# Performance work log

Measured on AMD Instinct MI355X. Metric: run time of the kernel, lower is better.

## Reference

```python
import jax, jax.numpy as jnp
import numpy as np


def setup_inputs() -> dict:
    key = jax.random.key(0)
    k1, k2, k3, k4 = jax.random.split(key, 4)
    B, T, S, D = 32, 512, 1024, 1024
    inp = jax.random.normal(k1, (B, T, D), dtype=jnp.float32)
    ctx = jax.random.normal(k2, (B, S, D), dtype=jnp.float32)
    W_in = jax.random.normal(k3, (D, D), dtype=jnp.float32) * (1.0 / np.sqrt(D))
    W_out = jax.random.normal(k4, (D, 2 * D), dtype=jnp.float32) * (1.0 / np.sqrt(2 * D))
    return {"input": inp, "context": ctx, "W_in": W_in, "W_out": W_out}


def reference(input, context, W_in, W_out):
    # GlobalAttention, attn_type='general', no mask, no coverage, tgt_len > 1.
    B, T, D = input.shape
    S = context.shape[1]
    # score: (W_in h_t) . h_s   -> [B, T, S]
    h_t = jnp.einsum('btd,ed->bte', input, W_in)           # linear_in (no bias)
    align = jnp.einsum('btd,bsd->bts', h_t, context)
    align_vectors = jax.nn.softmax(align, axis=-1)          # [B, T, S]
    # weighted sum of context
    c = jnp.einsum('bts,bsd->btd', align_vectors, context)  # [B, T, D]
    # concat [c, input] -> linear_out (no bias for 'general') -> tanh
    concat_c = jnp.concatenate([c, input], axis=-1)          # [B, T, 2D]
    attn_h = jnp.tanh(jnp.einsum('btf,df->btd', concat_c, W_out))
    # not one_step: transpose to [T, B, ...]
    attn_h = jnp.transpose(attn_h, (1, 0, 2))
    align_vectors = jnp.transpose(align_vectors, (1, 0, 2))
    return attn_h, align_vectors
```

## Files before the change

### kernel.cpp

```cpp
#include <hip/hip_runtime.h>
#include <hip/hip_bf16.h>


typedef short bf16x8 __attribute__((ext_vector_type(8)));
typedef float f32x4 __attribute__((ext_vector_type(4)));
typedef unsigned short us;

#define NB 32
#define NT_ 512
#define NS 1024
#define ND 1024

__device__ inline us f2bf(float x) {
  unsigned u = __float_as_uint(x);
  u += 0x7FFFu + ((u >> 16) & 1u);
  return (us)(u >> 16);
}
__device__ inline float bf2f(us h) { return __uint_as_float(((unsigned)h) << 16); }

__device__ inline void store_split(us* __restrict__ hi, us* __restrict__ lo, size_t idx, float v) {
  us h = f2bf(v);
  hi[idx] = h;
  lo[idx] = f2bf(v - bf2f(h));
}

__global__ void ga_split(const float* __restrict__ src, us* __restrict__ hi,
                         us* __restrict__ lo, long n) {
  long i0 = ((long)blockIdx.x * blockDim.x + threadIdx.x) * 4;
  long stride = (long)gridDim.x * blockDim.x * 4;
  for (long i = i0; i < n; i += stride) {
    float4 v = *reinterpret_cast<const float4*>(src + i);
    ushort4 h, l;
    h.x = f2bf(v.x); l.x = f2bf(v.x - bf2f(h.x));
    h.y = f2bf(v.y); l.y = f2bf(v.y - bf2f(h.y));
    h.z = f2bf(v.z); l.z = f2bf(v.z - bf2f(h.z));
    h.w = f2bf(v.w); l.w = f2bf(v.w - bf2f(h.w));
    *reinterpret_cast<ushort4*>(hi + i) = h;
    *reinterpret_cast<ushort4*>(lo + i) = l;
  }
}

__global__ void ga_cvt(const float* __restrict__ src, us* __restrict__ dst, long n) {
  long i0 = ((long)blockIdx.x * blockDim.x + threadIdx.x) * 4;
  long stride = (long)gridDim.x * blockDim.x * 4;
  for (long i = i0; i < n; i += stride) {
    float4 v = *reinterpret_cast<const float4*>(src + i);
    ushort4 h;
    h.x = f2bf(v.x); h.y = f2bf(v.y); h.z = f2bf(v.z); h.w = f2bf(v.w);
    *reinterpret_cast<ushort4*>(dst + i) = h;
  }
}

__global__ void ga_transpose_split(const float* __restrict__ ctx, us* __restrict__ tHi,
                                   us* __restrict__ tLo) {
  __shared__ float tile[64][65];
  int s0 = blockIdx.x << 6, d0 = blockIdx.y << 6, b = blockIdx.z;
  const float* src = ctx + (size_t)b * NS * ND;
  int tid = threadIdx.x;
#pragma unroll
  for (int i = 0; i < 16; ++i) {
    int lin = (i << 8) + tid;
    int r = lin >> 6, c = lin & 63;
    tile[r][c] = src[(size_t)(s0 + r) * ND + d0 + c];
  }
  __syncthreads();
  us* oH = tHi + (size_t)b * ND * NS;
  us* oL = tLo + (size_t)b * ND * NS;
#pragma unroll
  for (int i = 0; i < 16; ++i) {
    int lin = (i << 8) + tid;
    int dr = lin >> 6, sc = lin & 63;
    float v = tile[sc][dr];
    size_t o = (size_t)(d0 + dr) * NS + s0 + sc;
    us h = f2bf(v);
    oH[o] = h;
    oL[o] = f2bf(v - bf2f(h));
  }
}

__global__ __launch_bounds__(256) void ga_softmax(float* __restrict__ al,
                                                  us* __restrict__ pHi, us* __restrict__ pLo) {
  int row = blockIdx.x;
  int tid = threadIdx.x;
  float* p = al + (size_t)row * NS;
  float4 v = *reinterpret_cast<const float4*>(p + (tid << 2));
  float m = fmaxf(fmaxf(v.x, v.y), fmaxf(v.z, v.w));
#pragma unroll
  for (int off = 32; off; off >>= 1) m = fmaxf(m, __shfl_xor(m, off));
  __shared__ float rmax[4], rsum[4];
  int wv = tid >> 6, ln = tid & 63;
  if (ln == 0) rmax[wv] = m;
  __syncthreads();
  m = fmaxf(fmaxf(rmax[0], rmax[1]), fmaxf(rmax[2], rmax[3]));
  float4 e;
  e.x = __expf(v.x - m); e.y = __expf(v.y - m);
  e.z = __expf(v.z - m); e.w = __expf(v.w - m);
  float s = e.x + e.y + e.z + e.w;
#pragma unroll
  for (int off = 32; off; off >>= 1) s += __shfl_xor(s, off);
  if (ln == 0) rsum[wv] = s;
  __syncthreads();
  s = rsum[0] + rsum[1] + rsum[2] + rsum[3];
  float inv = 1.0f / s;
  e.x *= inv; e.y *= inv; e.z *= inv; e.w *= inv;
  *reinterpret_cast<float4*>(p + (tid << 2)) = e;
  int t = row >> 5, b = row & 31;
  size_t o = ((size_t)b * NT_ + t) * NS + (tid << 2);
  ushort4 h, l;
  h.x = f2bf(e.x); l.x = f2bf(e.x - bf2f(h.x));
  h.y = f2bf(e.y); l.y = f2bf(e.y - bf2f(h.y));
  h.z = f2bf(e.z); l.z = f2bf(e.z - bf2f(h.z));
  h.w = f2bf(e.w); l.w = f2bf(e.w - bf2f(h.w));
  *reinterpret_cast<ushort4*>(pHi + o) = h;
  *reinterpret_cast<ushort4*>(pLo + o) = l;
}

__device__ inline void gload16(const us* g, void* l) {
  __builtin_amdgcn_global_load_lds((const __attribute__((address_space(1))) unsigned int*)g,
                                   (__attribute__((address_space(3))) unsigned int*)l, 16, 0, 0);
}

__device__ inline f32x4 mfma16(bf16x8 a, bf16x8 b, f32x4 c) {
  return __builtin_amdgcn_mfma_f32_16x16x32_bf16(a, b, c, 0, 0, 0);
}


#define VM4 asm volatile("s_waitcnt vmcnt(4)" ::: "memory")
#define VM0 asm volatile("s_waitcnt vmcnt(0)" ::: "memory")

#define STG_A(T, H) do {                                                           \
    int s3_ = (T) >> 4;                                                            \
    const us* ga_ = (MODE == 3)                                                    \
        ? ((s3_ == 0) ? pA0 : (s3_ == 1) ? pA1 : (s3_ == 2) ? pA2 : pA3)           \
        : ((s3_ == 2) ? pA1 : pA0);                                                \
    const us* g_ = ga_ + ((long)((T) & 15) << 6) + ((H) ? aOff1 : aOff0);          \
    char* d_ = lb + (((T) & 1) << 16) + ((H) << 14) + (tid << 4);                  \
    gload16(g_, d_);                                                               \
    gload16(g_ + ald64, d_ + 8192);                                                \
  } while (0)

#define STG_B(T, H) do {                                                           \
    int s3_ = (T) >> 4;                                                            \
    const us* gb_ = (MODE == 3) ? ((s3_ >= 2) ? pB2 : pB0)                         \
                                : ((s3_ == 1) ? pB1 : pB0);                        \
    const us* g_ = gb_ + ((long)((T) & 15) << 6) + ((H) ? bOff1 : bOff0);          \
    char* d_ = lb + (((T) & 1) << 16) + 32768 + ((H) << 14) + (tid << 4);          \
    gload16(g_, d_);                                                               \
    gload16(g_ + bld64, d_ + 8192);                                                \
  } while (0)

#define RD_A(BP, QM) do {                                                          \
    const char* p_ = (BP) + aRd + ((QM) << 13);                                    \
    _Pragma("unroll") for (int m_ = 0; m_ < 4; ++m_) {                             \
      a[m_][0] = *(const bf16x8*)(p_ + (m_ << 11) + colx0);                        \
      a[m_][1] = *(const bf16x8*)(p_ + (m_ << 11) + colx1);                        \
    }                                                                              \
  } while (0)

#define RD_B(BP, ARR, QN) do {                                                     \
    const char* p_ = (BP) + bRd + ((QN) << 12);                                    \
    _Pragma("unroll") for (int n_ = 0; n_ < 2; ++n_) {                             \
      ARR[n_][0] = *(const bf16x8*)(p_ + (n_ << 11) + colx0);                      \
      ARR[n_][1] = *(const bf16x8*)(p_ + (n_ << 11) + colx1);                      \
    }                                                                              \
  } while (0)

#define MM(QM, QN, ARR)                                                            \
  _Pragma("unroll") for (int ks_ = 0; ks_ < 2; ++ks_)                              \
  _Pragma("unroll") for (int m_ = 0; m_ < 4; ++m_)                                 \
  _Pragma("unroll") for (int n_ = 0; n_ < 2; ++n_)                                 \
    acc[(QM) * 4 + m_][(QN) * 2 + n_] =                                            \
        mfma16(a[m_][ks_], ARR[n_][ks_], acc[(QM) * 4 + m_][(QN) * 2 + n_])

#define PHX(RDS, STGS, TAILV, QM, QN, ARR) do {                                    \
    RDS;                                                                           \
    STGS;                                                                          \
    __builtin_amdgcn_s_barrier();                                                  \
    asm volatile("s_waitcnt lgkmcnt(0)" ::: "memory");                             \
    __builtin_amdgcn_sched_barrier(0);                                             \
    __builtin_amdgcn_s_setprio(1);                                                 \
    MM(QM, QN, ARR);                                                               \
    __builtin_amdgcn_s_setprio(0);                                                 \
    TAILV;                                                                         \
    __builtin_amdgcn_s_barrier();                                                  \
  } while (0)

template <int MODE>
__global__ __launch_bounds__(512, 2) void ga_g8(
    const us* __restrict__ Ahi, const us* __restrict__ Alo,
    const us* __restrict__ A2hi, const us* __restrict__ A2lo,
    const us* __restrict__ Bhi, const us* __restrict__ Blo,
    void* __restrict__ out0, void* __restrict__ out1,
    int K, int lda, int ldb, long astride, long bstride) {
  __shared__ __align__(16) char lds[131072];
  char* lb = lds;
  const int NTILES = K >> 6;
  const int NIT = NTILES >> 1;
  const int tid = threadIdx.x;
  const int lane = tid & 63;
  const int fr = lane & 15;
  const int wv = tid >> 6;
  const int wr = wv >> 2, wc = wv & 3;
  const int rowA = blockIdx.x << 8, colB = blockIdx.y << 8;
  const int bz = blockIdx.z;

  const us* pA0 = Ahi + (size_t)bz * astride + (size_t)rowA * lda;
  const us* pA1 = Alo + (size_t)bz * astride + (size_t)rowA * lda;
  const us* pA2 = (MODE == 3) ? A2hi + (size_t)rowA * lda : nullptr;
  const us* pA3 = (MODE == 3) ? A2lo + (size_t)rowA * lda : nullptr;
  const us* pB0 = Bhi + (size_t)bz * bstride + (size_t)colB * ldb;
  const us* pB1 = (MODE == 3) ? nullptr : Blo + (size_t)bz * bstride + (size_t)colB * ldb;
  const us* pB2 = (MODE == 3) ? pB0 + 1024 : nullptr;

  const int arow = tid >> 3;
  const long swe = (long)(((tid & 7) ^ (arow & 7)) << 3);
  const long aOff0 = (long)arow * lda + swe;
  const long aOff1 = aOff0 + 128L * lda;
  const long ald64 = 64L * lda;
  const long bOff0 = (long)arow * ldb + swe;
  const long bOff1 = bOff0 + 128L * ldb;
  const long bld64 = 64L * ldb;

  const int l16 = ((lane >> 4) & 3) << 4;
  const int colx0 = l16 ^ ((fr & 7) << 4);
  const int colx1 = colx0 ^ 64;
  const int aRd = (wr << 14) + (fr << 7);
  const int bRd = 32768 + ((wc >> 1) << 14) + ((wc & 1) << 13) + (fr << 7);
  const char* B0P = lb;
  const char* B1P = lb + 65536;

  bf16x8 a[4][2], b0[2][2], b1[2][2];
  f32x4 zero = {0.f, 0.f, 0.f, 0.f};
  f32x4 acc[8][4];
#pragma unroll
  for (int i = 0; i < 8; ++i)
#pragma unroll
    for (int k = 0; k < 4; ++k) acc[i][k] = zero;

  STG_A(0, 0); STG_A(0, 1); STG_B(0, 0); STG_B(0, 1);
  STG_B(1, 0); STG_B(1, 1);
  VM4;
  __builtin_amdgcn_s_barrier();

  for (int i = 0; i < NIT - 1; ++i) {
    const int X = i << 1;
    PHX({ RD_A(B0P, 0); RD_B(B0P, b0, 0); }, STG_A(X + 1, 0), , 0, 0, b0);
    PHX(RD_B(B0P, b1, 1),                    STG_A(X + 1, 1), , 0, 1, b1);
    PHX(RD_A(B0P, 1),                        STG_B(X + 2, 0), , 1, 1, b1);
    PHX(,                                    STG_B(X + 2, 1), VM4, 1, 0, b0);
    PHX({ RD_A(B1P, 0); RD_B(B1P, b0, 0); }, STG_A(X + 2, 0), , 0, 0, b0);
    PHX(RD_B(B1P, b1, 1),                    STG_A(X + 2, 1), , 0, 1, b1);
    PHX(RD_A(B1P, 1),                        STG_B(X + 3, 0), , 1, 1, b1);
    PHX(,                                    STG_B(X + 3, 1), VM4, 1, 0, b0);
  }
  {
    const int X = NTILES - 2;
    PHX({ RD_A(B0P, 0); RD_B(B0P, b0, 0); }, STG_A(X + 1, 0), , 0, 0, b0);
    PHX(RD_B(B0P, b1, 1),                    STG_A(X + 1, 1), , 0, 1, b1);
    PHX(RD_A(B0P, 1), , , 1, 1, b1);
    PHX(, , VM0, 1, 0, b0);
    PHX({ RD_A(B1P, 0); RD_B(B1P, b0, 0); }, , , 0, 0, b0);
    PHX(RD_B(B1P, b1, 1), , , 0, 1, b1);
    PHX(RD_A(B1P, 1), , , 1, 1, b1);
    PHX(, , , 1, 0, b0);
  }

#pragma unroll
  for (int mf = 0; mf < 8; ++mf)
#pragma unroll
    for (int nf = 0; nf < 4; ++nf)
#pragma unroll
      for (int j = 0; j < 4; ++j) {
        int r = rowA + (wr << 7) + (mf << 4) + (((lane >> 4) & 3) << 2) + j;
        int c = colB + (wc << 6) + (nf << 4) + fr;
        float v = acc[mf][nf][j];
        if constexpr (MODE == 0) {
          store_split((us*)out0, (us*)out1, (size_t)r * 1024 + c, v);
        } else if constexpr (MODE == 1) {
          ((float*)out0)[((size_t)r * NB + bz) * NS + c] = v;
        } else if constexpr (MODE == 2) {
          store_split((us*)out0, (us*)out1, ((size_t)bz * 512 + r) * 1024 + c, v);
        } else {
          int bb = r >> 9, tt2 = r & 511;
          ((float*)out0)[((size_t)tt2 * NB + bb) * ND + c] = tanhf(v);
        }
      }
}

extern "C" void kernel_launch(void* const* d_in, const int* in_sizes, int n_in,
                              void* d_out, int out_size, void* d_ws, size_t ws_size,
                              hipStream_t stream) {
  (void)in_sizes; (void)n_in; (void)out_size; (void)ws_size;
  const float* inp = (const float*)d_in[0];
  const float* ctx = (const float*)d_in[1];
  const float* Win = (const float*)d_in[2];
  const float* Wout = (const float*)d_in[3];
  float* out = (float*)d_out;

  char* w = (char*)d_ws;
  us* ctx_hi  = (us*)(w + 0);
  us* c_hi    = (us*)(w + 0);
  us* c_lo    = (us*)(w + 33554432);
  us* ctx_lo  = (us*)(w + 67108864);
  us* p_hi    = (us*)(w + 67108864);
  us* p_lo    = (us*)(w + 100663296);
  us* in_hi   = (us*)(w + 134217728);
  us* in_lo   = (us*)(w + 167772160);
  us* h_hi    = (us*)(w + 201326592);
  us* h_lo    = (us*)(w + 234881024);
  us* ctxT_lo = (us*)(w + 201326592);
  us* win_hi  = (us*)(w + 268435456);
  us* win_lo  = (us*)(w + 270532608);
  us* wout_b  = (us*)(w + 272629760);

  us* ctxT_hi = (us*)d_out;
  float* alignOut = out + 16777216;

  ga_split<<<2048, 256, 0, stream>>>(inp, in_hi, in_lo, 16777216L);
  ga_split<<<2048, 256, 0, stream>>>(ctx, ctx_hi, ctx_lo, 33554432L);
  ga_split<<<512, 256, 0, stream>>>(Win, win_hi, win_lo, 1048576L);
  ga_cvt<<<512, 256, 0, stream>>>(Wout, wout_b, 2097152L);

  ga_g8<0><<<dim3(64, 4, 1), 512, 0, stream>>>(in_hi, in_lo, nullptr, nullptr,
                                               win_hi, win_lo, h_hi, h_lo,
                                               3072, 1024, 1024, 0L, 0L);
  ga_g8<1><<<dim3(2, 4, 32), 512, 0, stream>>>(h_hi, h_lo, nullptr, nullptr,
                                               ctx_hi, ctx_lo, alignOut, nullptr,
                                               3072, 1024, 1024, 524288L, 1048576L);
  ga_transpose_split<<<dim3(16, 16, 32), 256, 0, stream>>>(ctx, ctxT_hi, ctxT_lo);
  ga_softmax<<<16384, 256, 0, stream>>>(alignOut, p_hi, p_lo);
  ga_g8<2><<<dim3(2, 4, 32), 512, 0, stream>>>(p_hi, p_lo, nullptr, nullptr,
                                               ctxT_hi, ctxT_lo, c_hi, c_lo,
                                               3072, 1024, 1024, 524288L, 1048576L);
  ga_g8<3><<<dim3(64, 4, 1), 512, 0, stream>>>(c_hi, c_lo, in_hi, in_lo,
                                               wout_b, nullptr, out, nullptr,
                                               4096, 1024, 2048, 0L, 0L);
}
```

Before: 619.9 us.

## Restructure GEMM main loop to a single-barrier phase schedule with compile-time strides

Rewrites the 8-phase GEMM mainloop so each phase has one barrier instead of two. The B fragments are kept in registers across a whole k-tile and reloaded only at the tile boundary, and the global-to-LDS staging is moved after the MFMA block with vmcnt waits. Strides and tile counts become compile-time constants per mode, which cuts 64-bit address arithmetic and registers. Launch bounds change from 2 to 1 block per SM, trading occupancy for register headroom. The reordered LDS reads and writes add a risk of ordering hazards between buffers.

```diff
diff --git a/kernel.cpp b/kernel.cpp
--- a/kernel.cpp
+++ b/kernel.cpp
@@ -124,7 +124,6 @@
   return __builtin_amdgcn_mfma_f32_16x16x32_bf16(a, b, c, 0, 0, 0);
 }
 
-
 #define VM4 asm volatile("s_waitcnt vmcnt(4)" ::: "memory")
 #define VM0 asm volatile("s_waitcnt vmcnt(0)" ::: "memory")
 
@@ -133,27 +132,27 @@
     const us* ga_ = (MODE == 3)                                                    \
         ? ((s3_ == 0) ? pA0 : (s3_ == 1) ? pA1 : (s3_ == 2) ? pA2 : pA3)           \
         : ((s3_ == 2) ? pA1 : pA0);                                                \
-    const us* g_ = ga_ + ((long)((T) & 15) << 6) + ((H) ? aOff1 : aOff0);          \
+    const us* g_ = ga_ + (((T) & 15) << 6) + ((H) ? 131072 : 0) + aOff0;           \
     char* d_ = lb + (((T) & 1) << 16) + ((H) << 14) + (tid << 4);                  \
     gload16(g_, d_);                                                               \
-    gload16(g_ + ald64, d_ + 8192);                                                \
+    gload16(g_ + 65536, d_ + 8192);                                                \
   } while (0)
 
 #define STG_B(T, H) do {                                                           \
     int s3_ = (T) >> 4;                                                            \
     const us* gb_ = (MODE == 3) ? ((s3_ >= 2) ? pB2 : pB0)                         \
                                 : ((s3_ == 1) ? pB1 : pB0);                        \
-    const us* g_ = gb_ + ((long)((T) & 15) << 6) + ((H) ? bOff1 : bOff0);          \
+    const us* g_ = gb_ + (((T) & 15) << 6) + ((H) ? (LDB << 7) : 0) + bOff0;       \
     char* d_ = lb + (((T) & 1) << 16) + 32768 + ((H) << 14) + (tid << 4);          \
     gload16(g_, d_);                                                               \
-    gload16(g_ + bld64, d_ + 8192);                                                \
-  } while (0)
-
-#define RD_A(BP, QM) do {                                                          \
+    gload16(g_ + (LDB << 6), d_ + 8192);                                           \
+  } while (0)
+
+#define RD_A(BP, ARR, QM) do {                                                     \
     const char* p_ = (BP) + aRd + ((QM) << 13);                                    \
     _Pragma("unroll") for (int m_ = 0; m_ < 4; ++m_) {                             \
-      a[m_][0] = *(const bf16x8*)(p_ + (m_ << 11) + colx0);                        \
-      a[m_][1] = *(const bf16x8*)(p_ + (m_ << 11) + colx1);                        \
+      ARR[m_][0] = *(const bf16x8*)(p_ + (m_ << 11) + colx0);                      \
+      ARR[m_][1] = *(const bf16x8*)(p_ + (m_ << 11) + colx1);                      \
     }                                                                              \
   } while (0)
 
@@ -165,37 +164,34 @@
     }                                                                              \
   } while (0)
 
-#define MM(QM, QN, ARR)                                                            \
+#define MM(QM, QN, AA, BB)                                                         \
+  _Pragma("unroll") for (int m_ = 0; m_ < 4; ++m_)                                 \
   _Pragma("unroll") for (int ks_ = 0; ks_ < 2; ++ks_)                              \
-  _Pragma("unroll") for (int m_ = 0; m_ < 4; ++m_)                                 \
   _Pragma("unroll") for (int n_ = 0; n_ < 2; ++n_)                                 \
     acc[(QM) * 4 + m_][(QN) * 2 + n_] =                                            \
-        mfma16(a[m_][ks_], ARR[n_][ks_], acc[(QM) * 4 + m_][(QN) * 2 + n_])
-
-#define PHX(RDS, STGS, TAILV, QM, QN, ARR) do {                                    \
+        mfma16(AA[m_][ks_], BB[n_][ks_], acc[(QM) * 4 + m_][(QN) * 2 + n_])
+
+#define PH(RDS, MMQ, POST) do {                                                    \
+    __builtin_amdgcn_s_barrier();                                                  \
     RDS;                                                                           \
-    STGS;                                                                          \
-    __builtin_amdgcn_s_barrier();                                                  \
-    asm volatile("s_waitcnt lgkmcnt(0)" ::: "memory");                             \
-    __builtin_amdgcn_sched_barrier(0);                                             \
     __builtin_amdgcn_s_setprio(1);                                                 \
-    MM(QM, QN, ARR);                                                               \
+    MMQ;                                                                           \
     __builtin_amdgcn_s_setprio(0);                                                 \
-    TAILV;                                                                         \
-    __builtin_amdgcn_s_barrier();                                                  \
+    POST;                                                                          \
   } while (0)
 
 template <int MODE>
-__global__ __launch_bounds__(512, 2) void ga_g8(
+__global__ __launch_bounds__(512, 1) void ga_gb(
     const us* __restrict__ Ahi, const us* __restrict__ Alo,
     const us* __restrict__ A2hi, const us* __restrict__ A2lo,
     const us* __restrict__ Bhi, const us* __restrict__ Blo,
     void* __restrict__ out0, void* __restrict__ out1,
-    int K, int lda, int ldb, long astride, long bstride) {
+    long astride, long bstride) {
+  constexpr int LDB = (MODE == 3) ? 2048 : 1024;
+  constexpr int NT = (MODE == 3) ? 64 : 48;
+  constexpr int NIT = NT >> 1;
   __shared__ __align__(16) char lds[131072];
   char* lb = lds;
-  const int NTILES = K >> 6;
-  const int NIT = NTILES >> 1;
   const int tid = threadIdx.x;
   const int lane = tid & 63;
   const int fr = lane & 15;
@@ -204,32 +200,28 @@
   const int rowA = blockIdx.x << 8, colB = blockIdx.y << 8;
   const int bz = blockIdx.z;
 
-  const us* pA0 = Ahi + (size_t)bz * astride + (size_t)rowA * lda;
-  const us* pA1 = Alo + (size_t)bz * astride + (size_t)rowA * lda;
-  const us* pA2 = (MODE == 3) ? A2hi + (size_t)rowA * lda : nullptr;
-  const us* pA3 = (MODE == 3) ? A2lo + (size_t)rowA * lda : nullptr;
-  const us* pB0 = Bhi + (size_t)bz * bstride + (size_t)colB * ldb;
-  const us* pB1 = (MODE == 3) ? nullptr : Blo + (size_t)bz * bstride + (size_t)colB * ldb;
+  const us* pA0 = Ahi + (size_t)bz * astride + (size_t)rowA * 1024;
+  const us* pA1 = Alo + (size_t)bz * astride + (size_t)rowA * 1024;
+  const us* pA2 = (MODE == 3) ? A2hi + (size_t)rowA * 1024 : nullptr;
+  const us* pA3 = (MODE == 3) ? A2lo + (size_t)rowA * 1024 : nullptr;
+  const us* pB0 = Bhi + (size_t)bz * bstride + (size_t)colB * LDB;
+  const us* pB1 = (MODE == 3) ? nullptr : Blo + (size_t)bz * bstride + (size_t)colB * LDB;
   const us* pB2 = (MODE == 3) ? pB0 + 1024 : nullptr;
 
   const int arow = tid >> 3;
-  const long swe = (long)(((tid & 7) ^ (arow & 7)) << 3);
-  const long aOff0 = (long)arow * lda + swe;
-  const long aOff1 = aOff0 + 128L * lda;
-  const long ald64 = 64L * lda;
-  const long bOff0 = (long)arow * ldb + swe;
-  const long bOff1 = bOff0 + 128L * ldb;
-  const long bld64 = 64L * ldb;
+  const int swe = ((tid & 7) ^ (arow & 7)) << 3;
+  const int aOff0 = arow * 1024 + swe;
+  const int bOff0 = arow * LDB + swe;
 
   const int l16 = ((lane >> 4) & 3) << 4;
   const int colx0 = l16 ^ ((fr & 7) << 4);
   const int colx1 = colx0 ^ 64;
   const int aRd = (wr << 14) + (fr << 7);
   const int bRd = 32768 + ((wc >> 1) << 14) + ((wc & 1) << 13) + (fr << 7);
-  const char* B0P = lb;
-  const char* B1P = lb + 65536;
-
-  bf16x8 a[4][2], b0[2][2], b1[2][2];
+  const char* BUF0 = lb;
+  const char* BUF1 = lb + 65536;
+
+  bf16x8 a4[4][2], b0[2][2], b1[2][2];
   f32x4 zero = {0.f, 0.f, 0.f, 0.f};
   f32x4 acc[8][4];
 #pragma unroll
@@ -237,33 +229,34 @@
 #pragma unroll
     for (int k = 0; k < 4; ++k) acc[i][k] = zero;
 
-  STG_A(0, 0); STG_A(0, 1); STG_B(0, 0); STG_B(0, 1);
-  STG_B(1, 0); STG_B(1, 1);
-  VM4;
+  STG_B(0, 0); STG_B(0, 1); STG_A(0, 0); STG_A(0, 1);
+  STG_B(1, 0); STG_B(1, 1); STG_A(1, 0);
+  VM0;
   __builtin_amdgcn_s_barrier();
+  RD_B(BUF0, b0, 0); RD_B(BUF0, b1, 1);
 
   for (int i = 0; i < NIT - 1; ++i) {
     const int X = i << 1;
-    PHX({ RD_A(B0P, 0); RD_B(B0P, b0, 0); }, STG_A(X + 1, 0), , 0, 0, b0);
-    PHX(RD_B(B0P, b1, 1),                    STG_A(X + 1, 1), , 0, 1, b1);
-    PHX(RD_A(B0P, 1),                        STG_B(X + 2, 0), , 1, 1, b1);
-    PHX(,                                    STG_B(X + 2, 1), VM4, 1, 0, b0);
-    PHX({ RD_A(B1P, 0); RD_B(B1P, b0, 0); }, STG_A(X + 2, 0), , 0, 0, b0);
-    PHX(RD_B(B1P, b1, 1),                    STG_A(X + 2, 1), , 0, 1, b1);
-    PHX(RD_A(B1P, 1),                        STG_B(X + 3, 0), , 1, 1, b1);
-    PHX(,                                    STG_B(X + 3, 1), VM4, 1, 0, b0);
-  }
-  {
-    const int X = NTILES - 2;
-    PHX({ RD_A(B0P, 0); RD_B(B0P, b0, 0); }, STG_A(X + 1, 0), , 0, 0, b0);
-    PHX(RD_B(B0P, b1, 1),                    STG_A(X + 1, 1), , 0, 1, b1);
-    PHX(RD_A(B0P, 1), , , 1, 1, b1);
-    PHX(, , VM0, 1, 0, b0);
-    PHX({ RD_A(B1P, 0); RD_B(B1P, b0, 0); }, , , 0, 0, b0);
-    PHX(RD_B(B1P, b1, 1), , , 0, 1, b1);
-    PHX(RD_A(B1P, 1), , , 1, 1, b1);
-    PHX(, , , 1, 0, b0);
-  }
+    PH(RD_A(BUF0, a4, 0), MM(0, 0, a4, b0), { STG_A(X + 1, 1); VM4; });
+    PH(,                  MM(0, 1, a4, b1), { STG_B(X + 2, 0); VM4; });
+    PH(RD_A(BUF0, a4, 1), MM(1, 0, a4, b0), { STG_B(X + 2, 1); VM4; });
+    PH(,                  MM(1, 1, a4, b1),
+       { RD_B(BUF1, b0, 0); RD_B(BUF1, b1, 1); STG_A(X + 2, 0); VM4; });
+    PH(RD_A(BUF1, a4, 0), MM(0, 0, a4, b0), { STG_A(X + 2, 1); VM4; });
+    PH(,                  MM(0, 1, a4, b1), { STG_B(X + 3, 0); VM4; });
+    PH(RD_A(BUF1, a4, 1), MM(1, 0, a4, b0), { STG_B(X + 3, 1); VM4; });
+    PH(,                  MM(1, 1, a4, b1),
+       { RD_B(BUF0, b0, 0); RD_B(BUF0, b1, 1); STG_A(X + 3, 0); VM4; });
+  }
+  PH(RD_A(BUF0, a4, 0), MM(0, 0, a4, b0), { STG_A(NT - 1, 1); VM4; });
+  PH(,                  MM(0, 1, a4, b1), {});
+  PH(RD_A(BUF0, a4, 1), MM(1, 0, a4, b0), { VM0; });
+  PH(,                  MM(1, 1, a4, b1),
+     { RD_B(BUF1, b0, 0); RD_B(BUF1, b1, 1); });
+  PH(RD_A(BUF1, a4, 0), MM(0, 0, a4, b0), {});
+  PH(,                  MM(0, 1, a4, b1), {});
+  PH(RD_A(BUF1, a4, 1), MM(1, 0, a4, b0), {});
+  PH(,                  MM(1, 1, a4, b1), {});
 
 #pragma unroll
   for (int mf = 0; mf < 8; ++mf)
@@ -321,18 +314,16 @@
   ga_split<<<512, 256, 0, stream>>>(Win, win_hi, win_lo, 1048576L);
   ga_cvt<<<512, 256, 0, stream>>>(Wout, wout_b, 2097152L);
 
-  ga_g8<0><<<dim3(64, 4, 1), 512, 0, stream>>>(in_hi, in_lo, nullptr, nullptr,
-                                               win_hi, win_lo, h_hi, h_lo,
-                                               3072, 1024, 1024, 0L, 0L);
-  ga_g8<1><<<dim3(2, 4, 32), 512, 0, stream>>>(h_hi, h_lo, nullptr, nullptr,
+  ga_gb<0><<<dim3(64, 4, 1), 512, 0, stream>>>(in_hi, in_lo, nullptr, nullptr,
+                                               win_hi, win_lo, h_hi, h_lo, 0L, 0L);
+  ga_gb<1><<<dim3(2, 4, 32), 512, 0, stream>>>(h_hi, h_lo, nullptr, nullptr,
                                                ctx_hi, ctx_lo, alignOut, nullptr,
-                                               3072, 1024, 1024, 524288L, 1048576L);
+                                               524288L, 1048576L);
   ga_transpose_split<<<dim3(16, 16, 32), 256, 0, stream>>>(ctx, ctxT_hi, ctxT_lo);
   ga_softmax<<<16384, 256, 0, stream>>>(alignOut, p_hi, p_lo);
-  ga_g8<2><<<dim3(2, 4, 32), 512, 0, stream>>>(p_hi, p_lo, nullptr, nullptr,
+  ga_gb<2><<<dim3(2, 4, 32), 512, 0, stream>>>(p_hi, p_lo, nullptr, nullptr,
                                                ctxT_hi, ctxT_lo, c_hi, c_lo,
-                                               3072, 1024, 1024, 524288L, 1048576L);
-  ga_g8<3><<<dim3(64, 4, 1), 512, 0, stream>>>(c_hi, c_lo, in_hi, in_lo,
-                                               wout_b, nullptr, out, nullptr,
-                                               4096, 1024, 2048, 0L, 0L);
-}
+                                               524288L, 1048576L);
+  ga_gb<3><<<dim3(64, 4, 1), 512, 0, stream>>>(c_hi, c_lo, in_hi, in_lo,
+                                               wout_b, nullptr, out, nullptr, 0L, 0L);
+}
```

Result: no change. 613.4 us (-1.0%).
